# Optimization experiments

Measured on AMD Instinct MI355X. Metric: run time of the kernel, lower is better.

The kernel has to match this reference:

```python
import jax, jax.numpy as jnp
import numpy as np

HIDDEN = 300
N_NODES = 8192
N_CLAIM = 128
ALPHA = 0.5
TOPK_RATIO = 0.3
NUM_STEPS = 3


def setup_inputs() -> dict:
    key = jax.random.key(0)
    ks = jax.random.split(key, 10)
    H_e = jax.random.normal(ks[0], (N_NODES, HIDDEN), dtype=jnp.float32)
    H_c = jax.random.uniform(ks[1], (N_CLAIM, HIDDEN), dtype=jnp.float32)
    adj_e = jax.random.uniform(ks[2], (N_NODES, N_NODES), dtype=jnp.float32)
    # nn.Linear(hidden_dim, 1, bias=False) weight, stored as [hidden,1]
    W_score1 = jax.random.normal(ks[3], (HIDDEN, 1), dtype=jnp.float32) / np.sqrt(HIDDEN)
    # GGNN (hidden=1) GRU-style parameters, each scalar [1,1]
    Wz = jax.random.normal(ks[4], (1, 1), dtype=jnp.float32)
    Uz = jax.random.normal(ks[5], (1, 1), dtype=jnp.float32)
    Wr = jax.random.normal(ks[6], (1, 1), dtype=jnp.float32)
    Ur = jax.random.normal(ks[7], (1, 1), dtype=jnp.float32)
    Wh = jax.random.normal(ks[8], (1, 1), dtype=jnp.float32)
    Uh = jax.random.normal(ks[9], (1, 1), dtype=jnp.float32)
    return {"H_e": H_e, "H_c": H_c, "adj_e": adj_e, "W_score1": W_score1,
            "Wz": Wz, "Uz": Uz, "Wr": Wr, "Ur": Ur, "Wh": Wh, "Uh": Uh}


def _ggnn(h, adj, Wz, Uz, Wr, Ur, Wh, Uh):
    # Standard gated graph NN (Li et al.): message = adj @ h, GRU update. hidden=1.
    def step(h, _):
        a = adj @ h                               # [N,1] aggregated messages
        z = jax.nn.sigmoid(a @ Wz + h @ Uz)
        r = jax.nn.sigmoid(a @ Wr + h @ Ur)
        h_tilde = jnp.tanh(a @ Wh + (r * h) @ Uh)
        h_new = (1.0 - z) * h + z * h_tilde
        return h_new, None
    h_out, _ = jax.lax.scan(step, h, None, length=NUM_STEPS)
    return h_out


def reference(H_e, H_c, adj_e, W_score1, Wz, Uz, Wr, Ur, Wh, Uh):
    n = H_e.shape[0]
    # (11) self-redundancy
    score1 = H_e @ W_score1                       # [N,1]
    # (12) claim-relevance redundancy
    W = jax.nn.softmax(H_e @ H_c.T, axis=-1)      # [N, C]
    weighted_claim = W @ H_c                      # [N, hidden]
    relevance_sum = jnp.sum(weighted_claim, axis=-1, keepdims=True)
    score2 = -jnp.log(relevance_sum + 1e-10)
    # (13) combine
    score = ALPHA * score1 + (1.0 - ALPHA) * score2
    # (14) GGNN refinement over evidence graph
    S = _ggnn(score, adj_e, Wz, Uz, Wr, Ur, Wh, Uh)   # [N,1]
    # prune top-k highest-redundancy nodes (static k)
    k = int(TOPK_RATIO * n)
    order = jnp.argsort(S[:, 0])                  # ascending
    keep_idx = jnp.sort(order[: n - k])           # original node order, like H_e[keep_mask]
    keep_mask = jnp.zeros((n,), dtype=bool).at[keep_idx].set(True)
    H_e_refined = H_e[keep_idx]                   # [N-k, hidden]
    return H_e_refined, keep_mask
```

## Files before the change

kernel.cpp:

```cpp
#include <hip/hip_runtime.h>
#include <math.h>

#define N_NODES 8192
#define N_CLAIM 128
#define HIDDEN  300
#define KEEP    5735

__global__ __launch_bounds__(256) void prep_kernel(const float* __restrict__ Hc,
                                                   float* __restrict__ HcT,
                                                   float* __restrict__ scl) {
  int t = blockIdx.x * 256 + threadIdx.x;
  if (t < HIDDEN * N_CLAIM) {
    int k = t / N_CLAIM;
    int j = t - k * N_CLAIM;
    HcT[t] = Hc[j * HIDDEN + k];
  } else if (t < HIDDEN * N_CLAIM + N_CLAIM) {
    int j = t - HIDDEN * N_CLAIM;
    float s = 0.f;
    for (int k = 0; k < HIDDEN; ++k) s += Hc[j * HIDDEN + k];
    scl[j] = s;
  }
}

#define KC 50
__global__ __launch_bounds__(512) void score_kernel(
    const float* __restrict__ He, const float* __restrict__ HcT,
    const float* __restrict__ scl, const float* __restrict__ W1,
    float* __restrict__ score_out) {
  __shared__ float she[32][HIDDEN];
  __shared__ float shc[KC][N_CLAIM];
  const int tid  = threadIdx.x;
  const int wave = tid >> 6, lane = tid & 63;
  const int nb   = blockIdx.x * 32;

  {
    const float4* src4 = (const float4*)(He + (size_t)nb * HIDDEN);
    float4* dst4 = (float4*)&she[0][0];
    for (int i = tid; i < 32 * HIDDEN / 4; i += 512) dst4[i] = src4[i];
  }

  float a[4][2] = {{0.f,0.f},{0.f,0.f},{0.f,0.f},{0.f,0.f}};
  for (int k0 = 0; k0 < HIDDEN; k0 += KC) {
    __syncthreads();
    {
      const float4* c4 = (const float4*)(HcT + k0 * N_CLAIM);
      float4* d4 = (float4*)&shc[0][0];
      for (int i = tid; i < KC * N_CLAIM / 4; i += 512) d4[i] = c4[i];
    }
    __syncthreads();
    #pragma unroll 5
    for (int k = 0; k < KC; k += 2) {
      float2 ca = ((const float2*)shc[k])[lane];
      float2 cb = ((const float2*)shc[k + 1])[lane];
      #pragma unroll
      for (int n = 0; n < 4; ++n) {
        float2 h2v = ((const float2*)she[wave * 4 + n])[(k0 + k) >> 1];
        a[n][0] = fmaf(h2v.x, ca.x, fmaf(h2v.y, cb.x, a[n][0]));
        a[n][1] = fmaf(h2v.x, ca.y, fmaf(h2v.y, cb.y, a[n][1]));
      }
    }
  }

  float2 sc2 = ((const float2*)scl)[lane];
  float res[4];
  #pragma unroll
  for (int n = 0; n < 4; ++n) {
    float m = fmaxf(a[n][0], a[n][1]);
    #pragma unroll
    for (int s = 32; s; s >>= 1) m = fmaxf(m, __shfl_xor(m, s));
    float e0 = expf(a[n][0] - m), e1 = expf(a[n][1] - m);
    float den = e0 + e1, num = e0 * sc2.x + e1 * sc2.y;
    #pragma unroll
    for (int s = 32; s; s >>= 1) { den += __shfl_xor(den, s); num += __shfl_xor(num, s); }
    float s1 = 0.f;
    for (int k = lane; k < HIDDEN; k += 64) s1 = fmaf(she[wave * 4 + n][k], W1[k], s1);
    #pragma unroll
    for (int s = 32; s; s >>= 1) s1 += __shfl_xor(s1, s);
    res[n] = 0.5f * s1 + 0.5f * (-logf(num / den + 1e-10f));
  }
  if (lane == 0) {
    int n0 = nb + wave * 4;
    #pragma unroll
    for (int n = 0; n < 4; ++n) score_out[n0 + n] = res[n];
  }
}

__device__ inline float gru_update(float acc, float hi,
                                   float Wz, float Uz, float Wr, float Ur,
                                   float Wh, float Uh) {
  float z  = 1.f / (1.f + expf(-(acc * Wz + hi * Uz)));
  float r  = 1.f / (1.f + expf(-(acc * Wr + hi * Ur)));
  float ht = tanhf(acc * Wh + (r * hi) * Uh);
  return (1.f - z) * hi + z * ht;
}

__global__ __launch_bounds__(256) void ggnn_step1(
    const float* __restrict__ adj, const float* __restrict__ h_in,
    float* __restrict__ h_out, float* __restrict__ a_out,
    float* __restrict__ rowsum_out,
    const float* __restrict__ pWz, const float* __restrict__ pUz,
    const float* __restrict__ pWr, const float* __restrict__ pUr,
    const float* __restrict__ pWh, const float* __restrict__ pUh) {
  const int wave = threadIdx.x >> 6, lane = threadIdx.x & 63;
  const int row  = blockIdx.x * 4 + wave;
  const float4* __restrict__ a4 = (const float4*)(adj + (size_t)row * N_NODES);
  const float4* __restrict__ h4 = (const float4*)h_in;
  float acc = 0.f, rs = 0.f;
  #pragma unroll 8
  for (int it = 0; it < N_NODES / 256; ++it) {
    float4 a = a4[it * 64 + lane];
    float4 h = h4[it * 64 + lane];
    acc = fmaf(a.x, h.x, acc); acc = fmaf(a.y, h.y, acc);
    acc = fmaf(a.z, h.z, acc); acc = fmaf(a.w, h.w, acc);
    rs += (a.x + a.y) + (a.z + a.w);
  }
  #pragma unroll
  for (int s = 32; s; s >>= 1) { acc += __shfl_xor(acc, s); rs += __shfl_xor(rs, s); }
  if (lane == 0) {
    a_out[row] = acc;
    rowsum_out[row] = rs;
    h_out[row] = gru_update(acc, h_in[row], pWz[0], pUz[0], pWr[0], pUr[0], pWh[0], pUh[0]);
  }
}

__device__ inline unsigned int block_excl_scan_1024(unsigned int v, unsigned int* wsum,
                                                    int wave, int lane, int tid) {
  unsigned int sc = v;
  #pragma unroll
  for (int off = 1; off < 64; off <<= 1) {
    unsigned int o = __shfl_up(sc, off);
    if (lane >= off) sc += o;
  }
  __syncthreads();
  if (lane == 63) wsum[wave] = sc;
  __syncthreads();
  if (tid == 0) {
    unsigned int run = 0;
    for (int w = 0; w < 16; ++w) { unsigned int t = wsum[w]; wsum[w] = run; run += t; }
  }
  __syncthreads();
  return wsum[wave] + sc - v;
}

__device__ inline float block_dot_8192(const float* __restrict__ adjrow,
                                       const float4* __restrict__ h4,
                                       float* wred, int tid, int wave, int lane) {
  const float4* a4 = (const float4*)adjrow;
  float acc = 0.f;
  #pragma unroll
  for (int it = 0; it < 2; ++it) {
    int idx = tid + it * 1024;
    float4 a = a4[idx]; float4 h = h4[idx];
    acc = fmaf(a.x, h.x, fmaf(a.y, h.y, fmaf(a.z, h.z, fmaf(a.w, h.w, acc))));
  }
  #pragma unroll
  for (int s = 32; s; s >>= 1) acc += __shfl_xor(acc, s);
  if (lane == 0) wred[wave] = acc;
  __syncthreads();
  if (tid == 0) { float t = 0.f; for (int w = 0; w < 16; ++w) t += wred[w]; wred[0] = t; }
  __syncthreads();
  float r = wred[0];
  __syncthreads();
  return r;
}

__global__ __launch_bounds__(1024) void fused_refine_select(
    const float* __restrict__ h0, const float* __restrict__ h1,
    const float* __restrict__ a1, const float* __restrict__ rsum,
    const float* __restrict__ adj,
    float* __restrict__ mask_out, int* __restrict__ keep_idx,
    const float* __restrict__ pWz, const float* __restrict__ pUz,
    const float* __restrict__ pWr, const float* __restrict__ pUr,
    const float* __restrict__ pWh, const float* __restrict__ pUh) {
  __shared__ float h2s[N_NODES];
  __shared__ float a2s[N_NODES];
  __shared__ unsigned int keyz[N_NODES];
  __shared__ unsigned int hist[256];
  __shared__ unsigned int rbits[256];
  __shared__ unsigned int wsum[16];
  __shared__ float wred[16];
  __shared__ int s_same, s_eqc, s_nresc;
  __shared__ unsigned int sh_b, sh_newr, sh_prefix, sh_r;

  const int tid = threadIdx.x;
  const int wave = tid >> 6, lane = tid & 63;
  const int base = tid * 8;
  const float Wz = pWz[0], Uz = pUz[0], Wr = pWr[0], Ur = pUr[0];
  const float Wh = pWh[0], Uh = pUh[0];

  if (tid == 0) { s_same = 1; s_eqc = 1; s_nresc = 0; }
  if (tid < 256) rbits[tid] = 0u;
  __syncthreads();
  const float c0 = h1[0];
  {
    const float4* hc4 = (const float4*)h1;
    const float4* hp4 = (const float4*)h0;
    int same = 1, eqc = 1;
    for (int i = tid; i < N_NODES / 4; i += 1024) {
      float4 x = hc4[i], y = hp4[i];
      same &= (x.x == y.x) & (x.y == y.y) & (x.z == y.z) & (x.w == y.w);
      eqc  &= (x.x == c0) & (x.y == c0) & (x.z == c0) & (x.w == c0);
    }
    if (!same) atomicAnd(&s_same, 0);
    if (!eqc)  atomicAnd(&s_eqc, 0);
  }
  __syncthreads();
  {
    const int fsame = s_same, feqc = s_eqc;
    if (fsame) {
      for (int r = base; r < base + 8; ++r) {
        float acc = a1[r];
        a2s[r] = acc;
        h2s[r] = gru_update(acc, h1[r], Wz, Uz, Wr, Ur, Wh, Uh);
      }
    } else if (feqc) {
      for (int r = base; r < base + 8; ++r) {
        float acc = c0 * rsum[r];
        a2s[r] = acc;
        float zarg = acc * Wz + c0 * Uz;
        float wt   = acc * Wh;
        if (zarg <= -200.f) { h2s[r] = c0; }
        else if (zarg >= 200.f && fabsf(wt) - fabsf(c0 * Uh) >= 30.f) {
          h2s[r] = copysignf(1.f, wt);
        } else {
          atomicOr(&rbits[r >> 5], 1u << (r & 31)); atomicAdd(&s_nresc, 1);
        }
      }
    } else {
      for (int r = base; r < base + 8; ++r) {
        atomicOr(&rbits[r >> 5], 1u << (r & 31));
      }
      if (tid == 0) atomicAdd(&s_nresc, N_NODES);
    }
  }
  __syncthreads();
  if (s_nresc > 0) {
    for (int w = 0; w < 256; ++w) {
      unsigned int bits = rbits[w];
      while (bits) {
        int b = __ffs(bits) - 1; bits &= bits - 1;
        int i = w * 32 + b;
        float acc = block_dot_8192(adj + (size_t)i * N_NODES, (const float4*)h1,
                                   wred, tid, wave, lane);
        if (tid == 0) { a2s[i] = acc; h2s[i] = gru_update(acc, h1[i], Wz, Uz, Wr, Ur, Wh, Uh); }
      }
    }
  }
  __syncthreads();

  if (tid == 0) { s_same = 1; s_eqc = 1; s_nresc = 0; }
  if (tid < 256) rbits[tid] = 0u;
  __syncthreads();
  const float c1 = h2s[0];
  {
    const float4* hc4 = (const float4*)h2s;
    const float4* hp4 = (const float4*)h1;
    int same = 1, eqc = 1;
    for (int i = tid; i < N_NODES / 4; i += 1024) {
      float4 x = hc4[i], y = hp4[i];
      same &= (x.x == y.x) & (x.y == y.y) & (x.z == y.z) & (x.w == y.w);
      eqc  &= (x.x == c1) & (x.y == c1) & (x.z == c1) & (x.w == c1);
    }
    if (!same) atomicAnd(&s_same, 0);
    if (!eqc)  atomicAnd(&s_eqc, 0);
  }
  __syncthreads();
  {
    const int fsame = s_same, feqc = s_eqc;
    if (fsame) {
      for (int r = base; r < base + 8; ++r) {
        float acc = a2s[r];
        keyz[r] = __float_as_uint(gru_update(acc, h2s[r], Wz, Uz, Wr, Ur, Wh, Uh));
      }
    } else if (feqc) {
      for (int r = base; r < base + 8; ++r) {
        float acc = c1 * rsum[r];
        float zarg = acc * Wz + c1 * Uz;
        float wt   = acc * Wh;
        if (zarg <= -200.f) { keyz[r] = __float_as_uint(c1); }
        else if (zarg >= 200.f && fabsf(wt) - fabsf(c1 * Uh) >= 30.f) {
          keyz[r] = __float_as_uint(copysignf(1.f, wt));
        } else {
          atomicOr(&rbits[r >> 5], 1u << (r & 31)); atomicAdd(&s_nresc, 1);
        }
      }
    } else {
      for (int r = base; r < base + 8; ++r) {
        atomicOr(&rbits[r >> 5], 1u << (r & 31));
      }
      if (tid == 0) atomicAdd(&s_nresc, N_NODES);
    }
  }
  __syncthreads();
  if (s_nresc > 0) {
    for (int w = 0; w < 256; ++w) {
      unsigned int bits = rbits[w];
      while (bits) {
        int b = __ffs(bits) - 1; bits &= bits - 1;
        int i = w * 32 + b;
        float acc = block_dot_8192(adj + (size_t)i * N_NODES, (const float4*)h2s,
                                   wred, tid, wave, lane);
        if (tid == 0)
          keyz[i] = __float_as_uint(gru_update(acc, h2s[i], Wz, Uz, Wr, Ur, Wh, Uh));
      }
    }
  }
  __syncthreads();

  for (int i = tid; i < N_NODES; i += 1024) {
    unsigned int u = keyz[i];
    keyz[i] = (u & 0x80000000u) ? ~u : (u | 0x80000000u);
  }
  if (tid == 0) { sh_prefix = 0u; sh_r = KEEP; }
  __syncthreads();

  for (int pass = 0; pass < 4; ++pass) {
    const int shift = 24 - pass * 8;
    if (tid < 256) hist[tid] = 0u;
    __syncthreads();
    const unsigned int pref = sh_prefix;
    const unsigned int r    = sh_r;
    #pragma unroll
    for (int i = 0; i < 8; ++i) {
      unsigned int k = keyz[base + i];
      bool match = (pass == 0) || ((k >> (shift + 8)) == pref);
      unsigned int d = match ? ((k >> shift) & 255u) : 256u;
      unsigned long long m = ~0ull;
      #pragma unroll
      for (int b = 0; b < 9; ++b) {
        unsigned long long bal = __ballot((d >> b) & 1u);
        m &= ((d >> b) & 1u) ? bal : ~bal;
      }
      int leader = __ffsll((unsigned long long)m) - 1;
      if (lane == leader && d < 256u)
        atomicAdd(&hist[d], (unsigned int)__popcll(m));
    }
    __syncthreads();
    if (wave == 0) {
      unsigned int t0 = hist[lane * 4], t1 = hist[lane * 4 + 1];
      unsigned int t2 = hist[lane * 4 + 2], t3 = hist[lane * 4 + 3];
      unsigned int tot = t0 + t1 + t2 + t3;
      unsigned int sc = tot;
      #pragma unroll
      for (int off = 1; off < 64; off <<= 1) {
        unsigned int o = __shfl_up(sc, off);
        if (lane >= off) sc += o;
      }
      unsigned int e = sc - tot;
      unsigned int p0 = e + t0, p1 = p0 + t1, p2 = p1 + t2, p3 = p2 + t3;
      if (r > e  && r <= p0) { sh_b = lane * 4;     sh_newr = r - e;  }
      if (r > p0 && r <= p1) { sh_b = lane * 4 + 1; sh_newr = r - p0; }
      if (r > p1 && r <= p2) { sh_b = lane * 4 + 2; sh_newr = r - p1; }
      if (r > p2 && r <= p3) { sh_b = lane * 4 + 3; sh_newr = r - p2; }
    }
    __syncthreads();
    if (tid == 0) { sh_prefix = (pref << 8) | sh_b; sh_r = sh_newr; }
    __syncthreads();
  }
  const unsigned int Kk = sh_prefix;
  const unsigned int tk = sh_r;

  unsigned int eqc = 0;
  #pragma unroll
  for (int i = 0; i < 8; ++i) eqc += (keyz[base + i] == Kk) ? 1u : 0u;
  const unsigned int eqbase = block_excl_scan_1024(eqc, wsum, wave, lane, tid);

  unsigned int runeq = eqbase, kc = 0;
  #pragma unroll
  for (int i = 0; i < 8; ++i) {
    unsigned int k = keyz[base + i];
    bool kp;
    if (k == Kk) { kp = (runeq < tk); ++runeq; } else kp = (k < Kk);
    kc += kp ? 1u : 0u;
  }
  unsigned int pos = block_excl_scan_1024(kc, wsum, wave, lane, tid);

  runeq = eqbase;
  #pragma unroll
  for (int i = 0; i < 8; ++i) {
    unsigned int k = keyz[base + i];
    bool kp;
    if (k == Kk) { kp = (runeq < tk); ++runeq; } else kp = (k < Kk);
    mask_out[base + i] = kp ? 1.0f : 0.0f;
    if (kp) keep_idx[pos++] = base + i;
  }
}

__global__ __launch_bounds__(256) void gather_kernel(
    const float* __restrict__ He, const int* __restrict__ keep_idx,
    float* __restrict__ out) {
  int t = blockIdx.x * 256 + threadIdx.x;
  if (t >= KEEP * (HIDDEN / 4)) return;
  int p = t / (HIDDEN / 4);
  int c = t - p * (HIDDEN / 4);
  const float4* src = (const float4*)(He + (size_t)keep_idx[p] * HIDDEN);
  ((float4*)out)[t] = src[c];
}

extern "C" void kernel_launch(void* const* d_in, const int* in_sizes, int n_in,
                              void* d_out, int out_size, void* d_ws, size_t ws_size,
                              hipStream_t stream) {
  const float* He  = (const float*)d_in[0];
  const float* Hc  = (const float*)d_in[1];
  const float* adj = (const float*)d_in[2];
  const float* W1  = (const float*)d_in[3];
  const float* Wz  = (const float*)d_in[4];
  const float* Uz  = (const float*)d_in[5];
  const float* Wr  = (const float*)d_in[6];
  const float* Ur  = (const float*)d_in[7];
  const float* Wh  = (const float*)d_in[8];
  const float* Uh  = (const float*)d_in[9];
  float* out = (float*)d_out;

  float* ws   = (float*)d_ws;
  float* h0   = ws;
  float* h1   = ws + 1 * N_NODES;
  float* a1   = ws + 2 * N_NODES;
  float* rsum = ws + 3 * N_NODES;
  float* HcT  = ws + 4 * N_NODES;
  float* scl  = HcT + HIDDEN * N_CLAIM;
  int* keep_idx = (int*)(scl + N_CLAIM);

  float* mask_out = out + (size_t)KEEP * HIDDEN;

  prep_kernel        <<<(HIDDEN * N_CLAIM + N_CLAIM + 255) / 256, 256, 0, stream>>>(Hc, HcT, scl);
  score_kernel       <<<N_NODES / 32, 512, 0, stream>>>(He, HcT, scl, W1, h0);
  ggnn_step1         <<<N_NODES / 4, 256, 0, stream>>>(adj, h0, h1, a1, rsum,
                                                       Wz, Uz, Wr, Ur, Wh, Uh);
  fused_refine_select<<<1, 1024, 0, stream>>>(h0, h1, a1, rsum, adj, mask_out, keep_idx,
                                              Wz, Uz, Wr, Ur, Wh, Uh);
  gather_kernel      <<<(KEEP * (HIDDEN / 4) + 255) / 256, 256, 0, stream>>>(He, keep_idx, out);
}
```

Before: 125.0 us.

## Fuse claim prep into score kernel and run selection as last-block tail of GGNN step

Removes the separate Hc transpose/sum kernel by loading Hc directly into padded shared memory inside the score kernel and accumulating claim sums in-register. Merges the single-block refine/select kernel into the GGNN step-1 kernel using an atomic completion counter so the last finishing block performs the refinement and radix selection. Intermediate arrays move from shared to global memory and the tail now uses 256 threads instead of 1024, which reduces launch count at the cost of a narrower serial tail.

```diff
diff --git a/kernel.cpp b/kernel.cpp
--- a/kernel.cpp
+++ b/kernel.cpp
@@ -5,30 +5,17 @@
 #define N_CLAIM 128
 #define HIDDEN  300
 #define KEEP    5735
-
-__global__ __launch_bounds__(256) void prep_kernel(const float* __restrict__ Hc,
-                                                   float* __restrict__ HcT,
-                                                   float* __restrict__ scl) {
-  int t = blockIdx.x * 256 + threadIdx.x;
-  if (t < HIDDEN * N_CLAIM) {
-    int k = t / N_CLAIM;
-    int j = t - k * N_CLAIM;
-    HcT[t] = Hc[j * HIDDEN + k];
-  } else if (t < HIDDEN * N_CLAIM + N_CLAIM) {
-    int j = t - HIDDEN * N_CLAIM;
-    float s = 0.f;
-    for (int k = 0; k < HIDDEN; ++k) s += Hc[j * HIDDEN + k];
-    scl[j] = s;
-  }
-}
-
-#define KC 50
-__global__ __launch_bounds__(512) void score_kernel(
-    const float* __restrict__ He, const float* __restrict__ HcT,
-    const float* __restrict__ scl, const float* __restrict__ W1,
-    float* __restrict__ score_out) {
+#define KC      50
+#define SHCP    132
+
+__global__ __launch_bounds__(512) void score_prep_kernel(
+    const float* __restrict__ He, const float* __restrict__ Hc,
+    const float* __restrict__ W1, float* __restrict__ score_out,
+    unsigned int* __restrict__ done) {
+  if (blockIdx.x == 0 && threadIdx.x == 0) done[0] = 0u;
+
   __shared__ float she[32][HIDDEN];
-  __shared__ float shc[KC][N_CLAIM];
+  __shared__ float shc[KC][SHCP];
   const int tid  = threadIdx.x;
   const int wave = tid >> 6, lane = tid & 63;
   const int nb   = blockIdx.x * 32;
@@ -40,28 +27,32 @@
   }
 
   float a[4][2] = {{0.f,0.f},{0.f,0.f},{0.f,0.f},{0.f,0.f}};
+  float sA = 0.f, sB = 0.f;
   for (int k0 = 0; k0 < HIDDEN; k0 += KC) {
     __syncthreads();
-    {
-      const float4* c4 = (const float4*)(HcT + k0 * N_CLAIM);
-      float4* d4 = (float4*)&shc[0][0];
-      for (int i = tid; i < KC * N_CLAIM / 4; i += 512) d4[i] = c4[i];
+    for (int idx = tid; idx < N_CLAIM * (KC / 2); idx += 512) {
+      int j  = idx / (KC / 2);
+      int kk = idx - j * (KC / 2);
+      float2 v = *(const float2*)(Hc + j * HIDDEN + k0 + 2 * kk);
+      shc[2 * kk][j]     = v.x;
+      shc[2 * kk + 1][j] = v.y;
     }
     __syncthreads();
     #pragma unroll 5
     for (int k = 0; k < KC; k += 2) {
-      float2 ca = ((const float2*)shc[k])[lane];
-      float2 cb = ((const float2*)shc[k + 1])[lane];
+      float2 ca = ((const float2*)&shc[k][0])[lane];
+      float2 cb = ((const float2*)&shc[k + 1][0])[lane];
+      sA += ca.x + cb.x;
+      sB += ca.y + cb.y;
       #pragma unroll
       for (int n = 0; n < 4; ++n) {
-        float2 h2v = ((const float2*)she[wave * 4 + n])[(k0 + k) >> 1];
+        float2 h2v = ((const float2*)&she[wave * 4 + n][0])[(k0 + k) >> 1];
         a[n][0] = fmaf(h2v.x, ca.x, fmaf(h2v.y, cb.x, a[n][0]));
         a[n][1] = fmaf(h2v.x, ca.y, fmaf(h2v.y, cb.y, a[n][1]));
       }
     }
   }
 
-  float2 sc2 = ((const float2*)scl)[lane];
   float res[4];
   #pragma unroll
   for (int n = 0; n < 4; ++n) {
@@ -69,7 +60,7 @@
     #pragma unroll
     for (int s = 32; s; s >>= 1) m = fmaxf(m, __shfl_xor(m, s));
     float e0 = expf(a[n][0] - m), e1 = expf(a[n][1] - m);
-    float den = e0 + e1, num = e0 * sc2.x + e1 * sc2.y;
+    float den = e0 + e1, num = e0 * sA + e1 * sB;
     #pragma unroll
     for (int s = 32; s; s >>= 1) { den += __shfl_xor(den, s); num += __shfl_xor(num, s); }
     float s1 = 0.f;
@@ -94,37 +85,13 @@
   return (1.f - z) * hi + z * ht;
 }
 
-__global__ __launch_bounds__(256) void ggnn_step1(
-    const float* __restrict__ adj, const float* __restrict__ h_in,
-    float* __restrict__ h_out, float* __restrict__ a_out,
-    float* __restrict__ rowsum_out,
-    const float* __restrict__ pWz, const float* __restrict__ pUz,
-    const float* __restrict__ pWr, const float* __restrict__ pUr,
-    const float* __restrict__ pWh, const float* __restrict__ pUh) {
-  const int wave = threadIdx.x >> 6, lane = threadIdx.x & 63;
-  const int row  = blockIdx.x * 4 + wave;
-  const float4* __restrict__ a4 = (const float4*)(adj + (size_t)row * N_NODES);
-  const float4* __restrict__ h4 = (const float4*)h_in;
-  float acc = 0.f, rs = 0.f;
-  #pragma unroll 8
-  for (int it = 0; it < N_NODES / 256; ++it) {
-    float4 a = a4[it * 64 + lane];
-    float4 h = h4[it * 64 + lane];
-    acc = fmaf(a.x, h.x, acc); acc = fmaf(a.y, h.y, acc);
-    acc = fmaf(a.z, h.z, acc); acc = fmaf(a.w, h.w, acc);
-    rs += (a.x + a.y) + (a.z + a.w);
-  }
-  #pragma unroll
-  for (int s = 32; s; s >>= 1) { acc += __shfl_xor(acc, s); rs += __shfl_xor(rs, s); }
-  if (lane == 0) {
-    a_out[row] = acc;
-    rowsum_out[row] = rs;
-    h_out[row] = gru_update(acc, h_in[row], pWz[0], pUz[0], pWr[0], pUr[0], pWh[0], pUh[0]);
-  }
-}
-
-__device__ inline unsigned int block_excl_scan_1024(unsigned int v, unsigned int* wsum,
-                                                    int wave, int lane, int tid) {
+__device__ inline unsigned int mono_key(float f) {
+  unsigned int u = __float_as_uint(f);
+  return (u & 0x80000000u) ? ~u : (u | 0x80000000u);
+}
+
+__device__ inline unsigned int block_excl_scan_256(unsigned int v, unsigned int* wsum,
+                                                   int wave, int lane, int tid) {
   unsigned int sc = v;
   #pragma unroll
   for (int off = 1; off < 64; off <<= 1) {
@@ -136,67 +103,98 @@
   __syncthreads();
   if (tid == 0) {
     unsigned int run = 0;
-    for (int w = 0; w < 16; ++w) { unsigned int t = wsum[w]; wsum[w] = run; run += t; }
+    for (int w = 0; w < 4; ++w) { unsigned int t = wsum[w]; wsum[w] = run; run += t; }
   }
   __syncthreads();
   return wsum[wave] + sc - v;
 }
 
-__device__ inline float block_dot_8192(const float* __restrict__ adjrow,
-                                       const float4* __restrict__ h4,
-                                       float* wred, int tid, int wave, int lane) {
+__device__ inline float block_dot_256(const float* __restrict__ adjrow,
+                                      const float* __restrict__ hvec,
+                                      float* wred, int tid, int wave, int lane) {
   const float4* a4 = (const float4*)adjrow;
+  const float4* h4 = (const float4*)hvec;
   float acc = 0.f;
   #pragma unroll
-  for (int it = 0; it < 2; ++it) {
-    int idx = tid + it * 1024;
-    float4 a = a4[idx]; float4 h = h4[idx];
+  for (int it = 0; it < 8; ++it) {
+    int idx = tid + it * 256;
+    float4 a = a4[idx], h = h4[idx];
     acc = fmaf(a.x, h.x, fmaf(a.y, h.y, fmaf(a.z, h.z, fmaf(a.w, h.w, acc))));
   }
   #pragma unroll
   for (int s = 32; s; s >>= 1) acc += __shfl_xor(acc, s);
   if (lane == 0) wred[wave] = acc;
   __syncthreads();
-  if (tid == 0) { float t = 0.f; for (int w = 0; w < 16; ++w) t += wred[w]; wred[0] = t; }
+  if (tid == 0) { float t = 0.f; for (int w = 0; w < 4; ++w) t += wred[w]; wred[0] = t; }
   __syncthreads();
   float r = wred[0];
   __syncthreads();
   return r;
 }
 
-__global__ __launch_bounds__(1024) void fused_refine_select(
-    const float* __restrict__ h0, const float* __restrict__ h1,
-    const float* __restrict__ a1, const float* __restrict__ rsum,
-    const float* __restrict__ adj,
+__global__ __launch_bounds__(256) void step1_select_kernel(
+    const float* __restrict__ adj, const float* __restrict__ h0,
+    float* __restrict__ h1, float* __restrict__ a1, float* __restrict__ rsum,
+    float* __restrict__ h2g, float* __restrict__ a2g, unsigned int* __restrict__ keyg,
+    unsigned int* __restrict__ done,
     float* __restrict__ mask_out, int* __restrict__ keep_idx,
     const float* __restrict__ pWz, const float* __restrict__ pUz,
     const float* __restrict__ pWr, const float* __restrict__ pUr,
     const float* __restrict__ pWh, const float* __restrict__ pUh) {
-  __shared__ float h2s[N_NODES];
-  __shared__ float a2s[N_NODES];
-  __shared__ unsigned int keyz[N_NODES];
+  __shared__ unsigned int s_old;
   __shared__ unsigned int hist[256];
   __shared__ unsigned int rbits[256];
-  __shared__ unsigned int wsum[16];
-  __shared__ float wred[16];
+  __shared__ unsigned int wsum[4];
+  __shared__ float wred[4];
   __shared__ int s_same, s_eqc, s_nresc;
   __shared__ unsigned int sh_b, sh_newr, sh_prefix, sh_r;
 
   const int tid = threadIdx.x;
   const int wave = tid >> 6, lane = tid & 63;
-  const int base = tid * 8;
   const float Wz = pWz[0], Uz = pUz[0], Wr = pWr[0], Ur = pUr[0];
   const float Wh = pWh[0], Uh = pUh[0];
 
+  {
+    const int row = blockIdx.x * 4 + wave;
+    const float4* __restrict__ a4 = (const float4*)(adj + (size_t)row * N_NODES);
+    const float4* __restrict__ h4 = (const float4*)h0;
+    float acc = 0.f, rs = 0.f;
+    #pragma unroll 8
+    for (int it = 0; it < N_NODES / 256; ++it) {
+      float4 a = a4[it * 64 + lane];
+      float4 h = h4[it * 64 + lane];
+      acc = fmaf(a.x, h.x, acc); acc = fmaf(a.y, h.y, acc);
+      acc = fmaf(a.z, h.z, acc); acc = fmaf(a.w, h.w, acc);
+      rs += (a.x + a.y) + (a.z + a.w);
+    }
+    #pragma unroll
+    for (int s = 32; s; s >>= 1) { acc += __shfl_xor(acc, s); rs += __shfl_xor(rs, s); }
+    if (lane == 0) {
+      a1[row] = acc;
+      rsum[row] = rs;
+      h1[row] = gru_update(acc, h0[row], Wz, Uz, Wr, Ur, Wh, Uh);
+    }
+  }
+
+  __syncthreads();
+  if (tid == 0) {
+    __threadfence();
+    s_old = atomicAdd(done, 1u);
+  }
+  __syncthreads();
+  if (s_old != (unsigned)(N_NODES / 4 - 1)) return;
+  __threadfence();
+
+  const int base = tid * 32;
+
   if (tid == 0) { s_same = 1; s_eqc = 1; s_nresc = 0; }
-  if (tid < 256) rbits[tid] = 0u;
   __syncthreads();
   const float c0 = h1[0];
   {
     const float4* hc4 = (const float4*)h1;
     const float4* hp4 = (const float4*)h0;
     int same = 1, eqc = 1;
-    for (int i = tid; i < N_NODES / 4; i += 1024) {
+    for (int i = tid; i < N_NODES / 4; i += 256) {
       float4 x = hc4[i], y = hp4[i];
       same &= (x.x == y.x) & (x.y == y.y) & (x.z == y.z) & (x.w == y.w);
       eqc  &= (x.x == c0) & (x.y == c0) & (x.z == c0) & (x.w == c0);
@@ -206,32 +204,31 @@
   }
   __syncthreads();
   {
-    const int fsame = s_same, feqc = s_eqc;
-    if (fsame) {
-      for (int r = base; r < base + 8; ++r) {
+    unsigned int myresc = 0u;
+    if (s_same) {
+      for (int i = 0; i < 32; ++i) {
+        int r = base + i;
         float acc = a1[r];
-        a2s[r] = acc;
-        h2s[r] = gru_update(acc, h1[r], Wz, Uz, Wr, Ur, Wh, Uh);
-      }
-    } else if (feqc) {
-      for (int r = base; r < base + 8; ++r) {
+        a2g[r] = acc;
+        h2g[r] = gru_update(acc, h1[r], Wz, Uz, Wr, Ur, Wh, Uh);
+      }
+    } else if (s_eqc) {
+      for (int i = 0; i < 32; ++i) {
+        int r = base + i;
         float acc = c0 * rsum[r];
-        a2s[r] = acc;
+        a2g[r] = acc;
         float zarg = acc * Wz + c0 * Uz;
         float wt   = acc * Wh;
-        if (zarg <= -200.f) { h2s[r] = c0; }
-        else if (zarg >= 200.f && fabsf(wt) - fabsf(c0 * Uh) >= 30.f) {
-          h2s[r] = copysignf(1.f, wt);
-        } else {
-          atomicOr(&rbits[r >> 5], 1u << (r & 31)); atomicAdd(&s_nresc, 1);
-        }
+        if (zarg <= -200.f) h2g[r] = c0;
+        else if (zarg >= 200.f && fabsf(wt) - fabsf(c0 * Uh) >= 30.f)
+          h2g[r] = copysignf(1.f, wt);
+        else myresc |= (1u << i);
       }
     } else {
-      for (int r = base; r < base + 8; ++r) {
-        atomicOr(&rbits[r >> 5], 1u << (r & 31));
-      }
-      if (tid == 0) atomicAdd(&s_nresc, N_NODES);
-    }
+      myresc = 0xFFFFFFFFu;
+    }
+    rbits[tid] = myresc;
+    if (myresc) atomicAdd(&s_nresc, __popc(myresc));
   }
   __syncthreads();
   if (s_nresc > 0) {
@@ -240,23 +237,24 @@
       while (bits) {
         int b = __ffs(bits) - 1; bits &= bits - 1;
         int i = w * 32 + b;
-        float acc = block_dot_8192(adj + (size_t)i * N_NODES, (const float4*)h1,
-                                   wred, tid, wave, lane);
-        if (tid == 0) { a2s[i] = acc; h2s[i] = gru_update(acc, h1[i], Wz, Uz, Wr, Ur, Wh, Uh); }
+        float acc = block_dot_256(adj + (size_t)i * N_NODES, h1, wred, tid, wave, lane);
+        if (tid == 0) {
+          a2g[i] = acc;
+          h2g[i] = gru_update(acc, h1[i], Wz, Uz, Wr, Ur, Wh, Uh);
+        }
       }
     }
   }
   __syncthreads();
 
   if (tid == 0) { s_same = 1; s_eqc = 1; s_nresc = 0; }
-  if (tid < 256) rbits[tid] = 0u;
-  __syncthreads();
-  const float c1 = h2s[0];
-  {
-    const float4* hc4 = (const float4*)h2s;
+  __syncthreads();
+  const float c1 = h2g[0];
+  {
+    const float4* hc4 = (const float4*)h2g;
     const float4* hp4 = (const float4*)h1;
     int same = 1, eqc = 1;
-    for (int i = tid; i < N_NODES / 4; i += 1024) {
+    for (int i = tid; i < N_NODES / 4; i += 256) {
       float4 x = hc4[i], y = hp4[i];
       same &= (x.x == y.x) & (x.y == y.y) & (x.z == y.z) & (x.w == y.w);
       eqc  &= (x.x == c1) & (x.y == c1) & (x.z == c1) & (x.w == c1);
@@ -266,30 +264,28 @@
   }
   __syncthreads();
   {
-    const int fsame = s_same, feqc = s_eqc;
-    if (fsame) {
-      for (int r = base; r < base + 8; ++r) {
-        float acc = a2s[r];
-        keyz[r] = __float_as_uint(gru_update(acc, h2s[r], Wz, Uz, Wr, Ur, Wh, Uh));
-      }
-    } else if (feqc) {
-      for (int r = base; r < base + 8; ++r) {
+    unsigned int myresc = 0u;
+    if (s_same) {
+      for (int i = 0; i < 32; ++i) {
+        int r = base + i;
+        keyg[r] = mono_key(gru_update(a2g[r], h2g[r], Wz, Uz, Wr, Ur, Wh, Uh));
+      }
+    } else if (s_eqc) {
+      for (int i = 0; i < 32; ++i) {
+        int r = base + i;
         float acc = c1 * rsum[r];
         float zarg = acc * Wz + c1 * Uz;
         float wt   = acc * Wh;
-        if (zarg <= -200.f) { keyz[r] = __float_as_uint(c1); }
-        else if (zarg >= 200.f && fabsf(wt) - fabsf(c1 * Uh) >= 30.f) {
-          keyz[r] = __float_as_uint(copysignf(1.f, wt));
-        } else {
-          atomicOr(&rbits[r >> 5], 1u << (r & 31)); atomicAdd(&s_nresc, 1);
-        }
+        if (zarg <= -200.f) keyg[r] = mono_key(c1);
+        else if (zarg >= 200.f && fabsf(wt) - fabsf(c1 * Uh) >= 30.f)
+          keyg[r] = mono_key(copysignf(1.f, wt));
+        else myresc |= (1u << i);
       }
     } else {
-      for (int r = base; r < base + 8; ++r) {
-        atomicOr(&rbits[r >> 5], 1u << (r & 31));
-      }
-      if (tid == 0) atomicAdd(&s_nresc, N_NODES);
-    }
+      myresc = 0xFFFFFFFFu;
+    }
+    rbits[tid] = myresc;
+    if (myresc) atomicAdd(&s_nresc, __popc(myresc));
   }
   __syncthreads();
   if (s_nresc > 0) {
@@ -298,31 +294,32 @@
       while (bits) {
         int b = __ffs(bits) - 1; bits &= bits - 1;
         int i = w * 32 + b;
-        float acc = block_dot_8192(adj + (size_t)i * N_NODES, (const float4*)h2s,
-                                   wred, tid, wave, lane);
+        float acc = block_dot_256(adj + (size_t)i * N_NODES, h2g, wred, tid, wave, lane);
         if (tid == 0)
-          keyz[i] = __float_as_uint(gru_update(acc, h2s[i], Wz, Uz, Wr, Ur, Wh, Uh));
-      }
-    }
-  }
-  __syncthreads();
-
-  for (int i = tid; i < N_NODES; i += 1024) {
-    unsigned int u = keyz[i];
-    keyz[i] = (u & 0x80000000u) ? ~u : (u | 0x80000000u);
+          keyg[i] = mono_key(gru_update(acc, h2g[i], Wz, Uz, Wr, Ur, Wh, Uh));
+      }
+    }
+  }
+  __syncthreads();
+
+  unsigned int kv[32];
+  #pragma unroll
+  for (int q = 0; q < 8; ++q) {
+    uint4 t = ((const uint4*)keyg)[tid * 8 + q];
+    kv[q * 4 + 0] = t.x; kv[q * 4 + 1] = t.y; kv[q * 4 + 2] = t.z; kv[q * 4 + 3] = t.w;
   }
   if (tid == 0) { sh_prefix = 0u; sh_r = KEEP; }
   __syncthreads();
 
   for (int pass = 0; pass < 4; ++pass) {
     const int shift = 24 - pass * 8;
-    if (tid < 256) hist[tid] = 0u;
+    hist[tid] = 0u;
     __syncthreads();
     const unsigned int pref = sh_prefix;
     const unsigned int r    = sh_r;
     #pragma unroll
-    for (int i = 0; i < 8; ++i) {
-      unsigned int k = keyz[base + i];
+    for (int i = 0; i < 32; ++i) {
+      unsigned int k = kv[i];
       bool match = (pass == 0) || ((k >> (shift + 8)) == pref);
       unsigned int d = match ? ((k >> shift) & 255u) : 256u;
       unsigned long long m = ~0ull;
@@ -362,23 +359,23 @@
 
   unsigned int eqc = 0;
   #pragma unroll
-  for (int i = 0; i < 8; ++i) eqc += (keyz[base + i] == Kk) ? 1u : 0u;
-  const unsigned int eqbase = block_excl_scan_1024(eqc, wsum, wave, lane, tid);
+  for (int i = 0; i < 32; ++i) eqc += (kv[i] == Kk) ? 1u : 0u;
+  const unsigned int eqbase = block_excl_scan_256(eqc, wsum, wave, lane, tid);
 
   unsigned int runeq = eqbase, kc = 0;
   #pragma unroll
-  for (int i = 0; i < 8; ++i) {
-    unsigned int k = keyz[base + i];
+  for (int i = 0; i < 32; ++i) {
+    unsigned int k = kv[i];
     bool kp;
     if (k == Kk) { kp = (runeq < tk); ++runeq; } else kp = (k < Kk);
     kc += kp ? 1u : 0u;
   }
-  unsigned int pos = block_excl_scan_1024(kc, wsum, wave, lane, tid);
+  unsigned int pos = block_excl_scan_256(kc, wsum, wave, lane, tid);
 
   runeq = eqbase;
   #pragma unroll
-  for (int i = 0; i < 8; ++i) {
-    unsigned int k = keyz[base + i];
+  for (int i = 0; i < 32; ++i) {
+    unsigned int k = kv[i];
     bool kp;
     if (k == Kk) { kp = (runeq < tk); ++runeq; } else kp = (k < Kk);
     mask_out[base + i] = kp ? 1.0f : 0.0f;
@@ -417,17 +414,18 @@
   float* h1   = ws + 1 * N_NODES;
   float* a1   = ws + 2 * N_NODES;
   float* rsum = ws + 3 * N_NODES;
-  float* HcT  = ws + 4 * N_NODES;
-  float* scl  = HcT + HIDDEN * N_CLAIM;
-  int* keep_idx = (int*)(scl + N_CLAIM);
+  float* h2g  = ws + 4 * N_NODES;
+  float* a2g  = ws + 5 * N_NODES;
+  unsigned int* keyg = (unsigned int*)(ws + 6 * N_NODES);
+  int* keep_idx      = (int*)(ws + 7 * N_NODES);
+  unsigned int* done = (unsigned int*)(ws + 8 * N_NODES);
 
   float* mask_out = out + (size_t)KEEP * HIDDEN;
 
-  prep_kernel        <<<(HIDDEN * N_CLAIM + N_CLAIM + 255) / 256, 256, 0, stream>>>(Hc, HcT, scl);
-  score_kernel       <<<N_NODES / 32, 512, 0, stream>>>(He, HcT, scl, W1, h0);
-  ggnn_step1         <<<N_NODES / 4, 256, 0, stream>>>(adj, h0, h1, a1, rsum,
+  score_prep_kernel  <<<N_NODES / 32, 512, 0, stream>>>(He, Hc, W1, h0, done);
+  step1_select_kernel<<<N_NODES / 4, 256, 0, stream>>>(adj, h0, h1, a1, rsum,
+                                                       h2g, a2g, keyg, done,
+                                                       mask_out, keep_idx,
                                                        Wz, Uz, Wr, Ur, Wh, Uh);
-  fused_refine_select<<<1, 1024, 0, stream>>>(h0, h1, a1, rsum, adj, mask_out, keep_idx,
-                                              Wz, Uz, Wr, Ur, Wh, Uh);
   gather_kernel      <<<(KEEP * (HIDDEN / 4) + 255) / 256, 256, 0, stream>>>(He, keep_idx, out);
 }
```

New measurement: 228.1 us. 82.5% more time.
